# Performance work log

Measured on AMD Instinct MI355X. Metric: run time of the kernel, lower is better.

Reference implementation:

```python
import jax, jax.numpy as jnp
import numpy as np

N_QUBITS = 16
N_LAYERS = 3
N_STATES = 2 ** N_QUBITS


def setup_inputs() -> dict:
    key = jax.random.key(0)
    ks = jax.random.split(key, 6)
    B = 256
    return {
        "molecular_features": jax.random.normal(ks[0], (B, 100), jnp.float32),
        "rotation_params": jax.random.normal(ks[1], (N_LAYERS, N_QUBITS, 3), jnp.float32),
        "entangling_params": jax.random.normal(ks[2], (N_LAYERS, N_QUBITS - 1), jnp.float32),
        "W1": jax.random.normal(ks[3], (100, 64), jnp.float32) * 0.1,
        "b1": jnp.zeros((64,), jnp.float32),
        "W2": jax.random.normal(ks[4], (64, N_QUBITS), jnp.float32) * 0.1,
        "b2": jnp.zeros((N_QUBITS,), jnp.float32),
    }


def _apply_single_qubit(amp, q, M):
    # bit q occupies the 2^q place in the flat index -> reshape so it is its own axis
    B = amp.shape[0]
    a = amp.reshape(B, -1, 2, 2 ** q)  # (B, high, bit_q, low)
    out = jnp.einsum('bij,bhjl->bhil', M, a)
    return out.reshape(B, N_STATES)


def _apply_cnot(amp, control, target, p):
    # torch per-state loop is equivalent (reads come from OLD amplitudes, pair
    # written twice with identical symmetric values) to:
    #   new[s] = (1-p)*old[s] + p*old[s ^ (1<<target)]   if control bit of s is 1
    #   new[s] = old[s]                                  otherwise
    B = amp.shape[0]
    a = amp.reshape(B, -1, 2, 2 ** target)
    flipped = jnp.flip(a, axis=2).reshape(B, N_STATES)
    ctrl = ((jnp.arange(N_STATES) >> control) & 1).astype(bool)
    mixed = (1.0 - p) * amp + p * flipped
    return jnp.where(ctrl[None, :], mixed, amp)


def _forward(molecular_features, rotation_params, entangling_params, W1, b1, W2, b2):
    h = jnp.tanh(jax.nn.relu(molecular_features @ W1 + b1) @ W2 + b2)  # (B, n_qubits)
    B = molecular_features.shape[0]
    amp = jnp.zeros((B, N_STATES), jnp.complex64).at[:, 0].set(1.0)
    for layer in range(N_LAYERS):
        for q in range(N_QUBITS):
            ang = rotation_params[layer, q][None, :] * h[:, q][:, None]  # (B, 3)
            c = jnp.cos(0.5 * ang)
            s = jnp.sin(0.5 * ang)
            cx, cy, cz = c[:, 0], c[:, 1], c[:, 2]
            sx, sy, sz = s[:, 0], s[:, 1], s[:, 2]
            # matches the (non-unitary) torch rotation_matrix construction
            M = jnp.stack(
                [cx * cy * cz, -sx * sy * sz, sx * sy * cz, cx * cy * sz], axis=-1
            ).reshape(B, 2, 2).astype(jnp.complex64)
            amp = _apply_single_qubit(amp, q, M)
        for q in range(N_QUBITS - 1):
            p = jax.nn.sigmoid(entangling_params[layer, q])
            amp = _apply_cnot(amp, q, q + 1, p)
    return amp


def reference(molecular_features, rotation_params, entangling_params, W1, b1, W2, b2):
    return _forward(molecular_features, rotation_params, entangling_params, W1, b1, W2, b2)
```

## Files before the change

### kernel.cpp

```cpp
#include <hip/hip_runtime.h>
#include <math.h>

#define NQ 16
#define NLAYERS 3
#define NSTATES 65536
#define BATCH 256

__device__ __forceinline__ float rd(const float* __restrict__ p, int i, int n) {
    return p[i < n ? i : (n - 1)];
}

template <int I> struct IC { static constexpr int v = I; };

template <int I, int N, typename F>
__device__ __forceinline__ void sfor_i(F& f) {
    if constexpr (I < N) {
        f(IC<I>{});
        sfor_i<I + 1, N>(f);
    }
}
template <int N, typename F>
__device__ __forceinline__ void sfor(F&& f) { sfor_i<0, N>(f); }

__device__ __forceinline__ void mix2(float& a, float& b, float p) {
    float na = (1.f - p) * a + p * b;
    float nb = (1.f - p) * b + p * a;
    a = na; b = nb;
}
__device__ __forceinline__ void bf2(float& a0, float& a1, float4 m) {
    float n0 = m.x * a0 + m.y * a1;
    float n1 = m.z * a0 + m.w * a1;
    a0 = n0; a1 = n1;
}

__global__
__attribute__((amdgpu_flat_work_group_size(1024, 1024)))
void qsim(const float* __restrict__ x,
          const float* __restrict__ rot,
          const float* __restrict__ ent,
          const float* __restrict__ W1,
          const float* __restrict__ b1,
          const float* __restrict__ W2,
          const float* __restrict__ b2,
          float* __restrict__ out,
          long long out_floats,
          int nx, int nrot, int nent, int nW1, int nb1, int nW2, int nb2) {
    const int tid  = threadIdx.x;
    const int b    = blockIdx.x;
    const int lane = tid & 63;
    const int wave = tid >> 6;
    const int wq   = (tid >> 8) & 3;
    const int wv   = (tid >> 6) & 3;

    __shared__ float  ldsS[32 * 1024];
    __shared__ float  scr[4 * 1024];
    __shared__ float4 Mg[NLAYERS * NQ];
    __shared__ float  pg[NLAYERS * (NQ - 1)];
    __shared__ float  hidS[64];
    __shared__ float  hqS[16];

    sfor<32>([&](auto J) { ldsS[J.v * 1024 + tid] = 0.f; });

    if (tid < 64) {
        float s = rd(b1, tid, nb1);
        for (int k = 0; k < 100; k++)
            s = fmaf(rd(x, b * 100 + k, nx), rd(W1, k * 64 + tid, nW1), s);
        hidS[tid] = fmaxf(s, 0.f);
    } else if (tid >= 64 && tid < 64 + NLAYERS * (NQ - 1)) {
        int i = tid - 64;
        pg[i] = 1.f / (1.f + expf(-rd(ent, i, nent)));
    }
    __syncthreads();

    if (tid < 16) {
        float s = rd(b2, tid, nb2);
#pragma unroll
        for (int i = 0; i < 64; i++)
            s = fmaf(hidS[i], rd(W2, i * 16 + tid, nW2), s);
        hqS[tid] = tanhf(s);
    }
    __syncthreads();

    if (tid < NLAYERS * NQ) {
        int q = tid & 15;
        float hv = hqS[q];
        float a0 = 0.5f * rd(rot, tid * 3 + 0, nrot) * hv;
        float a1 = 0.5f * rd(rot, tid * 3 + 1, nrot) * hv;
        float a2 = 0.5f * rd(rot, tid * 3 + 2, nrot) * hv;
        float cx = cosf(a0), sx = sinf(a0);
        float cy = cosf(a1), sy = sinf(a1);
        float cz = cosf(a2), sz = sinf(a2);
        Mg[tid] = make_float4(cx * cy * cz, -(sx * sy * sz),
                              sx * sy * cz,  cx * cy * sz);
    }
    __syncthreads();

    float r[32];
    sfor<32>([&](auto J) { r[J.v] = 0.f; });
    if (tid == 0) r[0] = 1.f;

    for (int l = 0; l < NLAYERS; l++) {
#pragma unroll
        for (int q = 0; q < 6; q++) {
            float4 m = Mg[l * NQ + q];
            int bit = (tid >> q) & 1;
            float cown  = bit ? m.w : m.x;
            float cpart = bit ? m.z : m.y;
            sfor<4>([&](auto C) {
                sfor<8>([&](auto K) {
                    constexpr int j = C.v * 8 + K.v;
                    float part = __shfl_xor(r[j], 1 << q);
                    r[j] = cown * r[j] + cpart * part;
                });
                __builtin_amdgcn_sched_barrier(0);
            });
        }
        sfor<5>([&](auto QQ) {
            float4 m = Mg[l * NQ + 10 + QQ.v];
            sfor<32>([&](auto J) {
                constexpr int h = 1 << QQ.v;
                if constexpr (!(J.v & h)) bf2(r[J.v], r[J.v | h], m);
            });
        });
        sfor<4>([&](auto W) {
            float t[8];
            sfor<8>([&](auto K) { t[K.v] = ldsS[(W.v * 8 + K.v) * 1024 + tid]; });
#pragma unroll
            for (int q = 0; q < 6; q++) {
                float4 m = Mg[l * NQ + q];
                int bit = (tid >> q) & 1;
                float cown  = bit ? m.w : m.x;
                float cpart = bit ? m.z : m.y;
                sfor<8>([&](auto K) {
                    float part = __shfl_xor(t[K.v], 1 << q);
                    t[K.v] = cown * t[K.v] + cpart * part;
                });
                __builtin_amdgcn_sched_barrier(0);
            }
            sfor<3>([&](auto QQ) {
                float4 m = Mg[l * NQ + 10 + QQ.v];
                sfor<8>([&](auto K) {
                    constexpr int h = 1 << QQ.v;
                    if constexpr (!(K.v & h)) bf2(t[K.v], t[K.v | h], m);
                });
            });
            sfor<8>([&](auto K) { ldsS[(W.v * 8 + K.v) * 1024 + tid] = t[K.v]; });
        });
        {
            float4 m13 = Mg[l * NQ + 13];
            float4 m14 = Mg[l * NQ + 14];
            sfor<8>([&](auto J) {
                float t0 = ldsS[(J.v)      * 1024 + tid];
                float t1 = ldsS[(8 + J.v)  * 1024 + tid];
                float t2 = ldsS[(16 + J.v) * 1024 + tid];
                float t3 = ldsS[(24 + J.v) * 1024 + tid];
                bf2(t0, t1, m13); bf2(t2, t3, m13);
                bf2(t0, t2, m14); bf2(t1, t3, m14);
                ldsS[(J.v)      * 1024 + tid] = t0;
                ldsS[(8 + J.v)  * 1024 + tid] = t1;
                ldsS[(16 + J.v) * 1024 + tid] = t2;
                ldsS[(24 + J.v) * 1024 + tid] = t3;
            });
        }

        sfor<2>([&](auto B14) {
            float val[16];
            sfor<4>([&](auto J) {
                sfor<4>([&](auto V) {
                    scr[V.v * 1024 + tid] = r[B14.v * 16 + J.v * 4 + V.v];
                });
                __syncthreads();
                if (wq == J.v) {
                    sfor<16>([&](auto G) {
                        val[G.v] = scr[wv * 1024 + G.v * 64 + lane];
                    });
                }
                __syncthreads();
            });
            sfor<4>([&](auto Q) {
                float4 m = Mg[l * NQ + 6 + Q.v];
                sfor<16>([&](auto G) {
                    constexpr int h = 1 << Q.v;
                    if constexpr (!(G.v & h)) bf2(val[G.v], val[G.v | h], m);
                });
                __builtin_amdgcn_sched_barrier(0);
            });
            sfor<16>([&](auto G) { r[B14.v * 16 + G.v] = val[G.v]; });

            float vL[16];
            {
                const int srow = B14.v * 16 + wave;
                sfor<16>([&](auto G) {
                    vL[G.v] = ldsS[srow * 1024 + G.v * 64 + lane];
                });
            }
            sfor<4>([&](auto Q) {
                float4 m = Mg[l * NQ + 6 + Q.v];
                sfor<16>([&](auto G) {
                    constexpr int h = 1 << Q.v;
                    if constexpr (!(G.v & h)) bf2(vL[G.v], vL[G.v | h], m);
                });
                __builtin_amdgcn_sched_barrier(0);
            });
            {
                float4 m15 = Mg[l * NQ + 15];
                sfor<16>([&](auto G) { bf2(r[B14.v * 16 + G.v], vL[G.v], m15); });
            }
            __syncthreads();
            sfor<16>([&](auto G) {
                ldsS[(B14.v * 16 + G.v) * 1024 + tid] = vL[G.v];
            });
        });

#pragma unroll
        for (int c = 0; c < 5; c++) {
            float p = pg[l * (NQ - 1) + c];
            int ctl = (tid >> c) & 1;
            float pc = ctl ? p : 0.f;
            float qc = ctl ? (1.f - p) : 1.f;
            sfor<4>([&](auto C) {
                sfor<8>([&](auto K) {
                    constexpr int j = C.v * 8 + K.v;
                    float f = __shfl_xor(r[j], 1 << (c + 1));
                    r[j] = qc * r[j] + pc * f;
                });
                __builtin_amdgcn_sched_barrier(0);
            });
        }
        {
            float p = pg[l * (NQ - 1) + 5];
            int ctl = (tid >> 5) & 1;
            float pc = ctl ? p : 0.f;
            float qc = ctl ? (1.f - p) : 1.f;
            sfor<2>([&](auto B14) { sfor<16>([&](auto G) {
                if constexpr (!(G.v & 1)) {
                    constexpr int i0 = B14.v * 16 + G.v, i1 = i0 | 1;
                    float a = r[i0], c2 = r[i1];
                    r[i0] = qc * a + pc * c2;
                    r[i1] = qc * c2 + pc * a;
                }
            }); });
        }
        sfor<3>([&](auto CC) {
            float p = pg[l * (NQ - 1) + 6 + CC.v];
            sfor<2>([&](auto B14) { sfor<16>([&](auto G) {
                constexpr int cm = 1 << CC.v;
                constexpr int tm = 2 << CC.v;
                if constexpr ((G.v & cm) && !(G.v & tm))
                    mix2(r[B14.v * 16 + G.v], r[B14.v * 16 + (G.v | tm)], p);
            }); });
        });
        sfor<2>([&](auto B14) {
            float t[16];
            sfor<16>([&](auto G) { t[G.v] = ldsS[(B14.v * 16 + G.v) * 1024 + tid]; });
#pragma unroll
            for (int c = 0; c < 5; c++) {
                float p = pg[l * (NQ - 1) + c];
                int ctl = (tid >> c) & 1;
                float pc = ctl ? p : 0.f;
                float qc = ctl ? (1.f - p) : 1.f;
                sfor<2>([&](auto HB) {
                    sfor<8>([&](auto K) {
                        constexpr int g = HB.v * 8 + K.v;
                        float f = __shfl_xor(t[g], 1 << (c + 1));
                        t[g] = qc * t[g] + pc * f;
                    });
                    __builtin_amdgcn_sched_barrier(0);
                });
            }
            {
                float p = pg[l * (NQ - 1) + 5];
                int ctl = (tid >> 5) & 1;
                float pc = ctl ? p : 0.f;
                float qc = ctl ? (1.f - p) : 1.f;
                sfor<16>([&](auto G) {
                    if constexpr (!(G.v & 1)) {
                        float a = t[G.v], c2 = t[G.v | 1];
                        t[G.v]     = qc * a + pc * c2;
                        t[G.v | 1] = qc * c2 + pc * a;
                    }
                });
            }
            sfor<3>([&](auto CC) {
                float p = pg[l * (NQ - 1) + 6 + CC.v];
                sfor<16>([&](auto G) {
                    constexpr int cm = 1 << CC.v;
                    constexpr int tm = 2 << CC.v;
                    if constexpr ((G.v & cm) && !(G.v & tm))
                        mix2(t[G.v], t[G.v | tm], p);
                });
            });
            sfor<16>([&](auto G) { ldsS[(B14.v * 16 + G.v) * 1024 + tid] = t[G.v]; });
        });

        {
            float p9  = pg[l * (NQ - 1) + 9];
            int  cb9  = (tid >> 9) & 1;
            float pc9 = cb9 ? p9 : 0.f;
            float qc9 = cb9 ? (1.f - p9) : 1.f;

            sfor<2>([&](auto B14) {
                float val[16];
                sfor<4>([&](auto J) {
                    sfor<4>([&](auto V) {
                        scr[V.v * 1024 + tid] = r[B14.v * 16 + J.v * 4 + V.v];
                    });
                    __syncthreads();
                    if (wq == J.v) {
                        sfor<16>([&](auto H) {
                            val[H.v] = scr[wv * 1024 + H.v * 64 + lane];
                        });
                    }
                    __syncthreads();
                });
                sfor<16>([&](auto H) {
                    if constexpr (!(H.v & 1)) {
                        float a = val[H.v], c2 = val[H.v | 1];
                        val[H.v]     = qc9 * a + pc9 * c2;
                        val[H.v | 1] = qc9 * c2 + pc9 * a;
                    }
                });
                sfor<3>([&](auto CC) {
                    float p = pg[l * (NQ - 1) + 10 + CC.v];
                    sfor<16>([&](auto H) {
                        constexpr int cm = 1 << CC.v;
                        constexpr int tm = 2 << CC.v;
                        if constexpr ((H.v & cm) && !(H.v & tm))
                            mix2(val[H.v], val[H.v | tm], p);
                    });
                });
                sfor<16>([&](auto H) { r[B14.v * 16 + H.v] = val[H.v]; });

                float vL[16];
                {
                    const int srow = B14.v * 16 + wave;
                    sfor<16>([&](auto H) {
                        vL[H.v] = ldsS[srow * 1024 + H.v * 64 + lane];
                    });
                }
                sfor<16>([&](auto H) {
                    if constexpr (!(H.v & 1)) {
                        float a = vL[H.v], c2 = vL[H.v | 1];
                        vL[H.v]     = qc9 * a + pc9 * c2;
                        vL[H.v | 1] = qc9 * c2 + pc9 * a;
                    }
                });
                sfor<3>([&](auto CC) {
                    float p = pg[l * (NQ - 1) + 10 + CC.v];
                    sfor<16>([&](auto H) {
                        constexpr int cm = 1 << CC.v;
                        constexpr int tm = 2 << CC.v;
                        if constexpr ((H.v & cm) && !(H.v & tm))
                            mix2(vL[H.v], vL[H.v | tm], p);
                    });
                });
                __syncthreads();
                sfor<16>([&](auto H) {
                    ldsS[(B14.v * 16 + H.v) * 1024 + tid] = vL[H.v];
                });
            });
        }

        {
            float p13 = pg[l * (NQ - 1) + 13];
            sfor<8>([&](auto K) { mix2(r[8 + K.v], r[24 + K.v], p13); });
            sfor<8>([&](auto K) {
                float a = ldsS[(8 + K.v)  * 1024 + tid];
                float c2 = ldsS[(24 + K.v) * 1024 + tid];
                mix2(a, c2, p13);
                ldsS[(8 + K.v)  * 1024 + tid] = a;
                ldsS[(24 + K.v) * 1024 + tid] = c2;
            });
        }
        {
            float p14 = pg[l * (NQ - 1) + 14];
            sfor<16>([&](auto K) {
                float v = ldsS[(16 + K.v) * 1024 + tid];
                mix2(r[16 + K.v], v, p14);
                ldsS[(16 + K.v) * 1024 + tid] = v;
            });
        }
    }

    long long base = (long long)b * NSTATES;
    sfor<32>([&](auto J) {
        long long fi = base + (long long)(J.v * 1024) + tid;
        if (fi < out_floats) out[fi] = r[J.v];
    });
    sfor<32>([&](auto J) {
        long long fi = base + 32768LL + (long long)(J.v * 1024) + tid;
        float v = ldsS[J.v * 1024 + tid];
        if (fi < out_floats) out[fi] = v;
    });
}

extern "C" void kernel_launch(void* const* d_in, const int* in_sizes, int n_in,
                              void* d_out, int out_size, void* d_ws, size_t ws_size,
                              hipStream_t stream) {
    const float* x   = (const float*)d_in[0];
    const float* rot = (const float*)d_in[1];
    const float* ent = (const float*)d_in[2];
    const float* W1  = (const float*)d_in[3];
    const float* b1  = (const float*)d_in[4];
    const float* W2  = (const float*)d_in[5];
    const float* b2  = (const float*)d_in[6];

    qsim<<<BATCH, 1024, 0, stream>>>(x, rot, ent, W1, b1, W2, b2,
                                     (float*)d_out, (long long)out_size,
                                     in_sizes[0], in_sizes[1], in_sizes[2],
                                     in_sizes[3], in_sizes[4], in_sizes[5],
                                     in_sizes[6]);
}
```

Measured before the change: 244.7 us.

## Fuse gate stages across layers, skew LDS layout, and skip zero-half work in layer 0

Reorganizes the per-layer gate schedule. The previous layer's trailing CNOTs (13,14) are fused with the next layer's rotations on qubits 13/14 and 10-12. The LDS-resident half's qubit 0-5 rotations and CNOTs 0-4 run in one transposed pass using a skewed (row-rotated) LDS addressing to avoid bank conflicts. Register and LDS halves share one scratch transpose for qubits 6-9 and 15. Layer 0 skips work on the LDS half, which is known to be zero, and drops the initial LDS zero-fill. The final CNOTs are folded into the output stores. This removes LDS round trips and shuffle passes, at the cost of more complex control flow and an extra synchronization.

```diff
diff --git a/kernel.cpp b/kernel.cpp
--- a/kernel.cpp
+++ b/kernel.cpp
@@ -27,10 +27,19 @@
     float nb = (1.f - p) * b + p * a;
     a = na; b = nb;
 }
+__device__ __forceinline__ void mixc(float& a, float& b, float qc, float pc) {
+    float na = qc * a + pc * b;
+    float nb = qc * b + pc * a;
+    a = na; b = nb;
+}
 __device__ __forceinline__ void bf2(float& a0, float& a1, float4 m) {
     float n0 = m.x * a0 + m.y * a1;
     float n1 = m.z * a0 + m.w * a1;
     a0 = n0; a1 = n1;
+}
+
+__device__ __forceinline__ int ladr(int row, int col) {
+    return row * 1024 + ((col + row) & 1023);
 }
 
 __global__
@@ -59,8 +68,6 @@
     __shared__ float  hidS[64];
     __shared__ float  hqS[16];
 
-    sfor<32>([&](auto J) { ldsS[J.v * 1024 + tid] = 0.f; });
-
     if (tid < 64) {
         float s = rd(b1, tid, nb1);
         for (int k = 0; k < 100; k++)
@@ -100,6 +107,59 @@
     if (tid == 0) r[0] = 1.f;
 
     for (int l = 0; l < NLAYERS; l++) {
+        if (l > 0) {
+            float p13p = pg[(l - 1) * 15 + 13];
+            float p14p = pg[(l - 1) * 15 + 14];
+            sfor<8>([&](auto K) { mix2(r[8 + K.v], r[24 + K.v], p13p); });
+            float4 m13 = Mg[l * NQ + 13];
+            float4 m14 = Mg[l * NQ + 14];
+            sfor<8>([&](auto W) {
+                float t0 = ldsS[ladr(W.v,      tid)];
+                float t1 = ldsS[ladr(W.v + 8,  tid)];
+                float t2 = ldsS[ladr(W.v + 16, tid)];
+                float t3 = ldsS[ladr(W.v + 24, tid)];
+                mix2(t1, t3, p13p);
+                mix2(r[W.v + 16], t2, p14p);
+                mix2(r[W.v + 24], t3, p14p);
+                bf2(t0, t1, m13); bf2(t2, t3, m13);
+                bf2(t0, t2, m14); bf2(t1, t3, m14);
+                ldsS[ladr(W.v,      tid)] = t0;
+                ldsS[ladr(W.v + 8,  tid)] = t1;
+                ldsS[ladr(W.v + 16, tid)] = t2;
+                ldsS[ladr(W.v + 24, tid)] = t3;
+            });
+            sfor<8>([&](auto K) { bf2(r[K.v],      r[K.v + 8],  m13); });
+            sfor<8>([&](auto K) { bf2(r[K.v + 16], r[K.v + 24], m13); });
+            sfor<16>([&](auto K) { bf2(r[K.v], r[K.v + 16], m14); });
+            sfor<4>([&](auto W) {
+                float t[8];
+                sfor<8>([&](auto K) { t[K.v] = ldsS[ladr(W.v * 8 + K.v, tid)]; });
+                sfor<3>([&](auto QQ) {
+                    float4 m = Mg[l * NQ + 10 + QQ.v];
+                    sfor<8>([&](auto K) {
+                        constexpr int h = 1 << QQ.v;
+                        if constexpr (!(K.v & h)) bf2(t[K.v], t[K.v | h], m);
+                    });
+                });
+                sfor<8>([&](auto K) { ldsS[ladr(W.v * 8 + K.v, tid)] = t[K.v]; });
+            });
+            sfor<3>([&](auto QQ) {
+                float4 m = Mg[l * NQ + 10 + QQ.v];
+                sfor<32>([&](auto J) {
+                    constexpr int h = 1 << QQ.v;
+                    if constexpr (!(J.v & h)) bf2(r[J.v], r[J.v | h], m);
+                });
+            });
+        } else {
+            sfor<5>([&](auto QQ) {
+                float4 m = Mg[10 + QQ.v];
+                sfor<32>([&](auto J) {
+                    constexpr int h = 1 << QQ.v;
+                    if constexpr (!(J.v & h)) bf2(r[J.v], r[J.v | h], m);
+                });
+            });
+        }
+
 #pragma unroll
         for (int q = 0; q < 6; q++) {
             float4 m = Mg[l * NQ + q];
@@ -115,106 +175,9 @@
                 __builtin_amdgcn_sched_barrier(0);
             });
         }
-        sfor<5>([&](auto QQ) {
-            float4 m = Mg[l * NQ + 10 + QQ.v];
-            sfor<32>([&](auto J) {
-                constexpr int h = 1 << QQ.v;
-                if constexpr (!(J.v & h)) bf2(r[J.v], r[J.v | h], m);
-            });
-        });
-        sfor<4>([&](auto W) {
-            float t[8];
-            sfor<8>([&](auto K) { t[K.v] = ldsS[(W.v * 8 + K.v) * 1024 + tid]; });
-#pragma unroll
-            for (int q = 0; q < 6; q++) {
-                float4 m = Mg[l * NQ + q];
-                int bit = (tid >> q) & 1;
-                float cown  = bit ? m.w : m.x;
-                float cpart = bit ? m.z : m.y;
-                sfor<8>([&](auto K) {
-                    float part = __shfl_xor(t[K.v], 1 << q);
-                    t[K.v] = cown * t[K.v] + cpart * part;
-                });
-                __builtin_amdgcn_sched_barrier(0);
-            }
-            sfor<3>([&](auto QQ) {
-                float4 m = Mg[l * NQ + 10 + QQ.v];
-                sfor<8>([&](auto K) {
-                    constexpr int h = 1 << QQ.v;
-                    if constexpr (!(K.v & h)) bf2(t[K.v], t[K.v | h], m);
-                });
-            });
-            sfor<8>([&](auto K) { ldsS[(W.v * 8 + K.v) * 1024 + tid] = t[K.v]; });
-        });
-        {
-            float4 m13 = Mg[l * NQ + 13];
-            float4 m14 = Mg[l * NQ + 14];
-            sfor<8>([&](auto J) {
-                float t0 = ldsS[(J.v)      * 1024 + tid];
-                float t1 = ldsS[(8 + J.v)  * 1024 + tid];
-                float t2 = ldsS[(16 + J.v) * 1024 + tid];
-                float t3 = ldsS[(24 + J.v) * 1024 + tid];
-                bf2(t0, t1, m13); bf2(t2, t3, m13);
-                bf2(t0, t2, m14); bf2(t1, t3, m14);
-                ldsS[(J.v)      * 1024 + tid] = t0;
-                ldsS[(8 + J.v)  * 1024 + tid] = t1;
-                ldsS[(16 + J.v) * 1024 + tid] = t2;
-                ldsS[(24 + J.v) * 1024 + tid] = t3;
-            });
-        }
-
-        sfor<2>([&](auto B14) {
-            float val[16];
-            sfor<4>([&](auto J) {
-                sfor<4>([&](auto V) {
-                    scr[V.v * 1024 + tid] = r[B14.v * 16 + J.v * 4 + V.v];
-                });
-                __syncthreads();
-                if (wq == J.v) {
-                    sfor<16>([&](auto G) {
-                        val[G.v] = scr[wv * 1024 + G.v * 64 + lane];
-                    });
-                }
-                __syncthreads();
-            });
-            sfor<4>([&](auto Q) {
-                float4 m = Mg[l * NQ + 6 + Q.v];
-                sfor<16>([&](auto G) {
-                    constexpr int h = 1 << Q.v;
-                    if constexpr (!(G.v & h)) bf2(val[G.v], val[G.v | h], m);
-                });
-                __builtin_amdgcn_sched_barrier(0);
-            });
-            sfor<16>([&](auto G) { r[B14.v * 16 + G.v] = val[G.v]; });
-
-            float vL[16];
-            {
-                const int srow = B14.v * 16 + wave;
-                sfor<16>([&](auto G) {
-                    vL[G.v] = ldsS[srow * 1024 + G.v * 64 + lane];
-                });
-            }
-            sfor<4>([&](auto Q) {
-                float4 m = Mg[l * NQ + 6 + Q.v];
-                sfor<16>([&](auto G) {
-                    constexpr int h = 1 << Q.v;
-                    if constexpr (!(G.v & h)) bf2(vL[G.v], vL[G.v | h], m);
-                });
-                __builtin_amdgcn_sched_barrier(0);
-            });
-            {
-                float4 m15 = Mg[l * NQ + 15];
-                sfor<16>([&](auto G) { bf2(r[B14.v * 16 + G.v], vL[G.v], m15); });
-            }
-            __syncthreads();
-            sfor<16>([&](auto G) {
-                ldsS[(B14.v * 16 + G.v) * 1024 + tid] = vL[G.v];
-            });
-        });
-
 #pragma unroll
         for (int c = 0; c < 5; c++) {
-            float p = pg[l * (NQ - 1) + c];
+            float p = pg[l * 15 + c];
             int ctl = (tid >> c) & 1;
             float pc = ctl ? p : 0.f;
             float qc = ctl ? (1.f - p) : 1.f;
@@ -227,78 +190,101 @@
                 __builtin_amdgcn_sched_barrier(0);
             });
         }
+
+        if (l > 0) {
+            __syncthreads();
+            const int Rlow  = tid & 15;
+            const int Cbase = tid & 0x3F0;
+            const int bit4  = (tid >> 4) & 1;
+            const int bit5  = (tid >> 5) & 1;
+            sfor<2>([&](auto H) {
+                const int R    = H.v * 16 + Rlow;
+                const int base = R * 1024;
+                const int cb   = Cbase + R;
+                float v[16];
+                sfor<16>([&](auto J) { v[J.v] = ldsS[base + ((cb + J.v) & 1023)]; });
+                sfor<4>([&](auto Q) {
+                    float4 m = Mg[l * NQ + Q.v];
+                    sfor<16>([&](auto J) {
+                        constexpr int h = 1 << Q.v;
+                        if constexpr (!(J.v & h)) bf2(v[J.v], v[J.v | h], m);
+                    });
+                });
+                {
+                    float4 m = Mg[l * NQ + 4];
+                    float cown  = bit4 ? m.w : m.x;
+                    float cpart = bit4 ? m.z : m.y;
+                    sfor<2>([&](auto C) {
+                        sfor<8>([&](auto K) {
+                            constexpr int j = C.v * 8 + K.v;
+                            float part = __shfl_xor(v[j], 16);
+                            v[j] = cown * v[j] + cpart * part;
+                        });
+                        __builtin_amdgcn_sched_barrier(0);
+                    });
+                }
+                {
+                    float4 m = Mg[l * NQ + 5];
+                    float cown  = bit5 ? m.w : m.x;
+                    float cpart = bit5 ? m.z : m.y;
+                    sfor<2>([&](auto C) {
+                        sfor<8>([&](auto K) {
+                            constexpr int j = C.v * 8 + K.v;
+                            float part = __shfl_xor(v[j], 32);
+                            v[j] = cown * v[j] + cpart * part;
+                        });
+                        __builtin_amdgcn_sched_barrier(0);
+                    });
+                }
+                {
+                    float p = pg[l * 15 + 0];
+                    sfor<16>([&](auto J) {
+                        if constexpr ((J.v & 1) && !(J.v & 2)) mix2(v[J.v], v[J.v | 2], p);
+                    });
+                }
+                {
+                    float p = pg[l * 15 + 1];
+                    sfor<16>([&](auto J) {
+                        if constexpr ((J.v & 2) && !(J.v & 4)) mix2(v[J.v], v[J.v | 4], p);
+                    });
+                }
+                {
+                    float p = pg[l * 15 + 2];
+                    sfor<16>([&](auto J) {
+                        if constexpr ((J.v & 4) && !(J.v & 8)) mix2(v[J.v], v[J.v | 8], p);
+                    });
+                }
+                {
+                    float p = pg[l * 15 + 3];
+                    sfor<8>([&](auto K) {
+                        constexpr int j = 8 + K.v;
+                        float f = __shfl_xor(v[j], 16);
+                        v[j] = (1.f - p) * v[j] + p * f;
+                    });
+                    __builtin_amdgcn_sched_barrier(0);
+                }
+                {
+                    float p = pg[l * 15 + 4];
+                    float pc = bit4 ? p : 0.f;
+                    float qc = bit4 ? (1.f - p) : 1.f;
+                    sfor<2>([&](auto C) {
+                        sfor<8>([&](auto K) {
+                            constexpr int j = C.v * 8 + K.v;
+                            float f = __shfl_xor(v[j], 32);
+                            v[j] = qc * v[j] + pc * f;
+                        });
+                        __builtin_amdgcn_sched_barrier(0);
+                    });
+                }
+                sfor<16>([&](auto J) { ldsS[base + ((cb + J.v) & 1023)] = v[J.v]; });
+            });
+        }
+
         {
-            float p = pg[l * (NQ - 1) + 5];
-            int ctl = (tid >> 5) & 1;
-            float pc = ctl ? p : 0.f;
-            float qc = ctl ? (1.f - p) : 1.f;
-            sfor<2>([&](auto B14) { sfor<16>([&](auto G) {
-                if constexpr (!(G.v & 1)) {
-                    constexpr int i0 = B14.v * 16 + G.v, i1 = i0 | 1;
-                    float a = r[i0], c2 = r[i1];
-                    r[i0] = qc * a + pc * c2;
-                    r[i1] = qc * c2 + pc * a;
-                }
-            }); });
-        }
-        sfor<3>([&](auto CC) {
-            float p = pg[l * (NQ - 1) + 6 + CC.v];
-            sfor<2>([&](auto B14) { sfor<16>([&](auto G) {
-                constexpr int cm = 1 << CC.v;
-                constexpr int tm = 2 << CC.v;
-                if constexpr ((G.v & cm) && !(G.v & tm))
-                    mix2(r[B14.v * 16 + G.v], r[B14.v * 16 + (G.v | tm)], p);
-            }); });
-        });
-        sfor<2>([&](auto B14) {
-            float t[16];
-            sfor<16>([&](auto G) { t[G.v] = ldsS[(B14.v * 16 + G.v) * 1024 + tid]; });
-#pragma unroll
-            for (int c = 0; c < 5; c++) {
-                float p = pg[l * (NQ - 1) + c];
-                int ctl = (tid >> c) & 1;
-                float pc = ctl ? p : 0.f;
-                float qc = ctl ? (1.f - p) : 1.f;
-                sfor<2>([&](auto HB) {
-                    sfor<8>([&](auto K) {
-                        constexpr int g = HB.v * 8 + K.v;
-                        float f = __shfl_xor(t[g], 1 << (c + 1));
-                        t[g] = qc * t[g] + pc * f;
-                    });
-                    __builtin_amdgcn_sched_barrier(0);
-                });
-            }
-            {
-                float p = pg[l * (NQ - 1) + 5];
-                int ctl = (tid >> 5) & 1;
-                float pc = ctl ? p : 0.f;
-                float qc = ctl ? (1.f - p) : 1.f;
-                sfor<16>([&](auto G) {
-                    if constexpr (!(G.v & 1)) {
-                        float a = t[G.v], c2 = t[G.v | 1];
-                        t[G.v]     = qc * a + pc * c2;
-                        t[G.v | 1] = qc * c2 + pc * a;
-                    }
-                });
-            }
-            sfor<3>([&](auto CC) {
-                float p = pg[l * (NQ - 1) + 6 + CC.v];
-                sfor<16>([&](auto G) {
-                    constexpr int cm = 1 << CC.v;
-                    constexpr int tm = 2 << CC.v;
-                    if constexpr ((G.v & cm) && !(G.v & tm))
-                        mix2(t[G.v], t[G.v | tm], p);
-                });
-            });
-            sfor<16>([&](auto G) { ldsS[(B14.v * 16 + G.v) * 1024 + tid] = t[G.v]; });
-        });
-
-        {
-            float p9  = pg[l * (NQ - 1) + 9];
-            int  cb9  = (tid >> 9) & 1;
-            float pc9 = cb9 ? p9 : 0.f;
-            float qc9 = cb9 ? (1.f - p9) : 1.f;
-
+            float p5 = pg[l * 15 + 5];
+            int ctl5 = (tid >> 5) & 1;
+            float pc5 = ctl5 ? p5 : 0.f;
+            float qc5 = ctl5 ? (1.f - p5) : 1.f;
             sfor<2>([&](auto B14) {
                 float val[16];
                 sfor<4>([&](auto J) {
@@ -307,91 +293,125 @@
                     });
                     __syncthreads();
                     if (wq == J.v) {
-                        sfor<16>([&](auto H) {
-                            val[H.v] = scr[wv * 1024 + H.v * 64 + lane];
-                        });
+                        sfor<16>([&](auto G) { val[G.v] = scr[wv * 1024 + G.v * 64 + lane]; });
                     }
                     __syncthreads();
                 });
+                float vL[16];
+                if (l > 0) {
+                    const int srow = B14.v * 16 + wave;
+                    sfor<16>([&](auto G) { vL[G.v] = ldsS[ladr(srow, G.v * 64 + lane)]; });
+                } else {
+                    sfor<16>([&](auto G) { vL[G.v] = 0.f; });
+                }
+                sfor<4>([&](auto Q) {
+                    float4 m = Mg[l * NQ + 6 + Q.v];
+                    sfor<16>([&](auto G) {
+                        constexpr int h = 1 << Q.v;
+                        if constexpr (!(G.v & h)) {
+                            bf2(val[G.v], val[G.v | h], m);
+                            bf2(vL[G.v],  vL[G.v | h],  m);
+                        }
+                    });
+                });
+                {
+                    float4 m15 = Mg[l * NQ + 15];
+                    sfor<16>([&](auto G) { bf2(val[G.v], vL[G.v], m15); });
+                }
+                sfor<16>([&](auto G) {
+                    if constexpr (!(G.v & 1)) {
+                        mixc(val[G.v], val[G.v | 1], qc5, pc5);
+                        mixc(vL[G.v],  vL[G.v | 1],  qc5, pc5);
+                    }
+                });
+                sfor<3>([&](auto CC) {
+                    float p = pg[l * 15 + 6 + CC.v];
+                    sfor<16>([&](auto G) {
+                        constexpr int cm = 1 << CC.v;
+                        constexpr int tm = 2 << CC.v;
+                        if constexpr ((G.v & cm) && !(G.v & tm)) {
+                            mix2(val[G.v], val[G.v | tm], p);
+                            mix2(vL[G.v],  vL[G.v | tm],  p);
+                        }
+                    });
+                });
+                __syncthreads();
+                sfor<16>([&](auto G) { ldsS[ladr(B14.v * 16 + G.v, tid)] = vL[G.v]; });
+                sfor<16>([&](auto G) { r[B14.v * 16 + G.v] = val[G.v]; });
+            });
+        }
+
+        {
+            float p9 = pg[l * 15 + 9];
+            int ctl9 = (tid >> 9) & 1;
+            float pc9 = ctl9 ? p9 : 0.f;
+            float qc9 = ctl9 ? (1.f - p9) : 1.f;
+            sfor<2>([&](auto B14) {
+                float val[16];
+                sfor<4>([&](auto J) {
+                    sfor<4>([&](auto V) {
+                        scr[V.v * 1024 + tid] = r[B14.v * 16 + J.v * 4 + V.v];
+                    });
+                    __syncthreads();
+                    if (wq == J.v) {
+                        sfor<16>([&](auto H) { val[H.v] = scr[wv * 1024 + H.v * 64 + lane]; });
+                    }
+                    __syncthreads();
+                });
+                float vL[16];
+                {
+                    const int srow = B14.v * 16 + wave;
+                    sfor<16>([&](auto H) { vL[H.v] = ldsS[ladr(srow, H.v * 64 + lane)]; });
+                }
                 sfor<16>([&](auto H) {
                     if constexpr (!(H.v & 1)) {
-                        float a = val[H.v], c2 = val[H.v | 1];
-                        val[H.v]     = qc9 * a + pc9 * c2;
-                        val[H.v | 1] = qc9 * c2 + pc9 * a;
+                        mixc(val[H.v], val[H.v | 1], qc9, pc9);
+                        mixc(vL[H.v],  vL[H.v | 1],  qc9, pc9);
                     }
                 });
                 sfor<3>([&](auto CC) {
-                    float p = pg[l * (NQ - 1) + 10 + CC.v];
+                    float p = pg[l * 15 + 10 + CC.v];
                     sfor<16>([&](auto H) {
                         constexpr int cm = 1 << CC.v;
                         constexpr int tm = 2 << CC.v;
-                        if constexpr ((H.v & cm) && !(H.v & tm))
+                        if constexpr ((H.v & cm) && !(H.v & tm)) {
                             mix2(val[H.v], val[H.v | tm], p);
-                    });
-                });
+                            mix2(vL[H.v],  vL[H.v | tm],  p);
+                        }
+                    });
+                });
+                __syncthreads();
+                sfor<16>([&](auto H) { ldsS[ladr(B14.v * 16 + H.v, tid)] = vL[H.v]; });
                 sfor<16>([&](auto H) { r[B14.v * 16 + H.v] = val[H.v]; });
-
-                float vL[16];
-                {
-                    const int srow = B14.v * 16 + wave;
-                    sfor<16>([&](auto H) {
-                        vL[H.v] = ldsS[srow * 1024 + H.v * 64 + lane];
-                    });
-                }
-                sfor<16>([&](auto H) {
-                    if constexpr (!(H.v & 1)) {
-                        float a = vL[H.v], c2 = vL[H.v | 1];
-                        vL[H.v]     = qc9 * a + pc9 * c2;
-                        vL[H.v | 1] = qc9 * c2 + pc9 * a;
-                    }
-                });
-                sfor<3>([&](auto CC) {
-                    float p = pg[l * (NQ - 1) + 10 + CC.v];
-                    sfor<16>([&](auto H) {
-                        constexpr int cm = 1 << CC.v;
-                        constexpr int tm = 2 << CC.v;
-                        if constexpr ((H.v & cm) && !(H.v & tm))
-                            mix2(vL[H.v], vL[H.v | tm], p);
-                    });
-                });
-                __syncthreads();
-                sfor<16>([&](auto H) {
-                    ldsS[(B14.v * 16 + H.v) * 1024 + tid] = vL[H.v];
-                });
-            });
-        }
-
-        {
-            float p13 = pg[l * (NQ - 1) + 13];
-            sfor<8>([&](auto K) { mix2(r[8 + K.v], r[24 + K.v], p13); });
-            sfor<8>([&](auto K) {
-                float a = ldsS[(8 + K.v)  * 1024 + tid];
-                float c2 = ldsS[(24 + K.v) * 1024 + tid];
-                mix2(a, c2, p13);
-                ldsS[(8 + K.v)  * 1024 + tid] = a;
-                ldsS[(24 + K.v) * 1024 + tid] = c2;
-            });
-        }
-        {
-            float p14 = pg[l * (NQ - 1) + 14];
-            sfor<16>([&](auto K) {
-                float v = ldsS[(16 + K.v) * 1024 + tid];
-                mix2(r[16 + K.v], v, p14);
-                ldsS[(16 + K.v) * 1024 + tid] = v;
-            });
-        }
-    }
-
-    long long base = (long long)b * NSTATES;
-    sfor<32>([&](auto J) {
-        long long fi = base + (long long)(J.v * 1024) + tid;
-        if (fi < out_floats) out[fi] = r[J.v];
-    });
-    sfor<32>([&](auto J) {
-        long long fi = base + 32768LL + (long long)(J.v * 1024) + tid;
-        float v = ldsS[J.v * 1024 + tid];
-        if (fi < out_floats) out[fi] = v;
-    });
+            });
+            __syncthreads();
+        }
+    }
+
+    {
+        float p13 = pg[2 * 15 + 13];
+        float p14 = pg[2 * 15 + 14];
+        sfor<8>([&](auto K) { mix2(r[8 + K.v], r[24 + K.v], p13); });
+        long long base = (long long)b * NSTATES;
+        sfor<8>([&](auto W) {
+            float t0 = ldsS[ladr(W.v,      tid)];
+            float t1 = ldsS[ladr(W.v + 8,  tid)];
+            float t2 = ldsS[ladr(W.v + 16, tid)];
+            float t3 = ldsS[ladr(W.v + 24, tid)];
+            mix2(t1, t3, p13);
+            mix2(r[W.v + 16], t2, p14);
+            mix2(r[W.v + 24], t3, p14);
+            long long fb = base + 32768LL + (long long)(W.v * 1024) + tid;
+            if (fb             < out_floats) out[fb]             = t0;
+            if (fb + 8  * 1024 < out_floats) out[fb + 8  * 1024] = t1;
+            if (fb + 16 * 1024 < out_floats) out[fb + 16 * 1024] = t2;
+            if (fb + 24 * 1024 < out_floats) out[fb + 24 * 1024] = t3;
+        });
+        sfor<32>([&](auto J) {
+            long long fi = base + (long long)(J.v * 1024) + tid;
+            if (fi < out_floats) out[fi] = r[J.v];
+        });
+    }
 }
 
 extern "C" void kernel_launch(void* const* d_in, const int* in_sizes, int n_in,
```

Result: slower. 267.9 us (+9.5%).
